# Performance work log

Measured on AMD Instinct MI355X. Metric: run time of the kernel, lower is better.

The kernel has to match this reference:

```python
import jax, jax.numpy as jnp
import numpy as np

D_IN = 1024
D_OUT = 1024


def setup_inputs() -> dict:
    key = jax.random.key(0)
    kx, kq, kk, kv = jax.random.split(key, 4)
    B, S = 4, 2048
    scale = 1.0 / np.sqrt(D_IN)
    return {
        "x": jax.random.normal(kx, (B, S, D_IN), dtype=jnp.float32),
        "Wq": jax.random.normal(kq, (D_IN, D_OUT), dtype=jnp.float32) * scale,
        "Wk": jax.random.normal(kk, (D_IN, D_OUT), dtype=jnp.float32) * scale,
        "Wv": jax.random.normal(kv, (D_IN, D_OUT), dtype=jnp.float32) * scale,
    }


def reference(x, Wq, Wk, Wv):
    # x: [B, S, D_in]; single-head causal attention (dropout=0 -> identity)
    q = jnp.einsum("bsd,de->bse", x, Wq)
    k = jnp.einsum("bsd,de->bse", x, Wk)
    v = jnp.einsum("bsd,de->bse", x, Wv)
    S = x.shape[1]
    d_k = k.shape[-1]
    scores = jnp.einsum("bqe,bke->bqk", q, k) / jnp.sqrt(jnp.float32(d_k))
    causal = jnp.tril(jnp.ones((S, S), dtype=bool))  # True = keep
    scores = jnp.where(causal, scores, -jnp.inf)
    weights = jax.nn.softmax(scores, axis=-1)
    return jnp.einsum("bqk,bke->bqe", weights, v)
```

## Files before the change

### kernel.cpp

```cpp
#include <hip/hip_runtime.h>

typedef unsigned short u16;
typedef __bf16 bf16x8_v __attribute__((ext_vector_type(8)));
typedef float f32x4 __attribute__((ext_vector_type(4)));

__device__ __forceinline__ u16 f2bf(float f) {
    unsigned u = __float_as_uint(f);
    unsigned r = u + 0x7fffu + ((u >> 16) & 1u);
    return (u16)(r >> 16);
}
__device__ __forceinline__ float bf2f(u16 h) {
    return __uint_as_float(((unsigned)h) << 16);
}

__device__ __forceinline__ void gll16(const u16* g, u16* l) {
    __builtin_amdgcn_global_load_lds(
        (const __attribute__((address_space(1))) void*)g,
        (__attribute__((address_space(3))) void*)l, 16, 0, 0);
}

#define EXP_SHIFT 12.0f

__device__ __forceinline__ float* srow_ptr(u16* Sb, int b, int i) {
    return (float*)((char*)Sb + (size_t)b * 8388608 +
                    ((i >> 9) << 12) + 2048 + ((size_t)(i & 511) << 2));
}

__global__ __launch_bounds__(256) void k_prep(const float* __restrict__ x,
                                              const float* __restrict__ Wq,
                                              const float* __restrict__ Wk,
                                              const float* __restrict__ Wv,
                                              u16* __restrict__ xb,
                                              u16* __restrict__ Wt3,
                                              float* __restrict__ out,
                                              u16* __restrict__ Sb) {
    __shared__ float tile[32][33];
    const int bid = blockIdx.x, tid = threadIdx.x;
    if (bid < 4096) {
        int i = (bid * 256 + tid) * 8;
        float4 a = *(const float4*)(x + i);
        float4 bb = *(const float4*)(x + i + 4);
        union { int4 p; u16 h[8]; } o;
        o.h[0] = f2bf(a.x);  o.h[1] = f2bf(a.y);  o.h[2] = f2bf(a.z);  o.h[3] = f2bf(a.w);
        o.h[4] = f2bf(bb.x); o.h[5] = f2bf(bb.y); o.h[6] = f2bf(bb.z); o.h[7] = f2bf(bb.w);
        *(int4*)(xb + i) = o.p;
    } else if (bid < 7168) {
        const int w = bid - 4096;
        const int z = w >> 10, rem = w & 1023;
        const int bx = rem & 31, by = rem >> 5;
        const float* W = (z == 0) ? Wq : (z == 1) ? Wk : Wv;
        u16* Wt = Wt3 + (size_t)z * 1024 * 1024;
        const int tx = tid & 31, ty = tid >> 5;
#pragma unroll
        for (int r = 0; r < 4; ++r)
            tile[ty + r * 8][tx] = W[(by * 32 + ty + r * 8) * 1024 + bx * 32 + tx];
        __syncthreads();
#pragma unroll
        for (int r = 0; r < 4; ++r)
            Wt[(bx * 32 + ty + r * 8) * 1024 + by * 32 + tx] =
                f2bf(tile[tx][ty + r * 8]);
    } else if (bid < 8192) {
        const int c = bid - 7168;
        int4 z4 = {0, 0, 0, 0};
        const int q0 = c * 1024 + tid * 4;
#pragma unroll
        for (int k = 0; k < 4; ++k) {
            const int q = q0 + k;
            const int b = q >> 18, off = q & 262143;
            *(int4*)(out + (size_t)b * 2097152 + 1048576 + (size_t)off * 4) = z4;
        }
    } else {
        const int chunk = tid >> 7;
        const int t = tid & 127;
#pragma unroll
        for (int c = 0; c < 8; ++c) {
            const int cc = c * 2 + chunk;
            char* p = (char*)Sb + (size_t)(cc >> 2) * 8388608 +
                      ((cc & 3) << 12) + 2048;
            int4 z4 = {0, 0, 0, 0};
            *(int4*)(p + t * 16) = z4;
        }
    }
}

__device__ __forceinline__ void gemm_core_nt(const u16* __restrict__ A,
                                             const u16* __restrict__ B,
                                             int lda, int ldb, int kLen,
                                             u16* smem, f32x4 acc[4][4]) {
    u16* As = smem;
    u16* Bs = smem + 128 * 64;
    const int tid = threadIdx.x;
    const int wave = tid >> 6;
    const int lane = tid & 63;
    const int rowA = tid >> 3;
    const int kcs  = (tid & 7) ^ (rowA & 7);
    const int row16 = lane & 15;
    const int quad = lane >> 4;
    const int sw = row16 & 7;
    const int wm = (wave >> 1) * 64;
    const int wn = (wave & 1) * 64;

#pragma unroll
    for (int i = 0; i < 4; ++i)
#pragma unroll
        for (int j = 0; j < 4; ++j) {
            f32x4 z = {0.f, 0.f, 0.f, 0.f};
            acc[i][j] = z;
        }

    const u16* Ag[4]; const u16* Bg[4];
    u16 *AsB[4], *BsB[4];
#pragma unroll
    for (int u = 0; u < 4; ++u) {
        Ag[u] = A + (size_t)(u * 32 + rowA) * lda + kcs * 8;
        Bg[u] = B + (size_t)(u * 32 + rowA) * ldb + kcs * 8;
        AsB[u] = As + (u * 256 + wave * 64) * 8;
        BsB[u] = Bs + (u * 256 + wave * 64) * 8;
    }

    const int ktiles = kLen >> 6;
    for (int kt = 0; kt < ktiles; ++kt) {
        __syncthreads();
#pragma unroll
        for (int u = 0; u < 4; ++u) gll16(Ag[u] + kt * 64, AsB[u]);
#pragma unroll
        for (int u = 0; u < 4; ++u) gll16(Bg[u] + kt * 64, BsB[u]);
        __syncthreads();
#pragma unroll
        for (int h = 0; h < 2; ++h) {
            bf16x8_v af[4], bfv[4];
            const int cp = (h * 4 + quad);
#pragma unroll
            for (int i = 0; i < 4; ++i)
                af[i] = *(const bf16x8_v*)(As + (wm + i * 16 + row16) * 64 +
                                           (cp ^ sw) * 8);
#pragma unroll
            for (int j = 0; j < 4; ++j)
                bfv[j] = *(const bf16x8_v*)(Bs + (wn + j * 16 + row16) * 64 +
                                            (cp ^ sw) * 8);
#pragma unroll
            for (int i = 0; i < 4; ++i)
#pragma unroll
                for (int j = 0; j < 4; ++j)
                    acc[i][j] = __builtin_amdgcn_mfma_f32_16x16x32_bf16(
                        af[i], bfv[j], acc[i][j], 0, 0, 0);
        }
    }
}

__device__ __forceinline__ void epi_bf16(const f32x4 acc[4][4], u16* smem,
                                         u16* __restrict__ g, int ldg) {
    const int tid = threadIdx.x;
    const int wave = tid >> 6, lane = tid & 63;
    const int row16 = lane & 15, quad = lane >> 4;
    u16* Ts = smem + wave * 2048;
#pragma unroll
    for (int jh = 0; jh < 2; ++jh) {
#pragma unroll
        for (int i = 0; i < 4; ++i)
#pragma unroll
            for (int jj = 0; jj < 2; ++jj) {
                const int j = jh * 2 + jj;
#pragma unroll
                for (int r = 0; r < 4; ++r)
                    Ts[(i * 16 + quad * 4 + r) * 32 + jj * 16 + row16] =
                        f2bf(acc[i][j][r]);
            }
#pragma unroll
        for (int s = 0; s < 4; ++s) {
            const int row = s * 16 + (lane >> 2);
            int4 val = *(const int4*)(Ts + row * 32 + (lane & 3) * 8);
            *(int4*)(g + (size_t)row * ldg + jh * 32 + (lane & 3) * 8) = val;
        }
    }
}

__device__ __forceinline__ void epi_vt(const f32x4 acc[4][4], u16* smem,
                                       u16* __restrict__ Vt, int m0w, int n0w) {
    const int tid = threadIdx.x;
    const int wave = tid >> 6, lane = tid & 63;
    const int row16 = lane & 15, quad = lane >> 4;
    const int b = m0w >> 11;
    const int sBase = m0w & 2047;
    u16* Ts = smem + wave * 4608;
#pragma unroll
    for (int p = 0; p < 2; ++p) {
#pragma unroll
        for (int i = 0; i < 4; ++i)
#pragma unroll
            for (int jj = 0; jj < 2; ++jj) {
                const int j = p * 2 + jj;
                union { unsigned long long d; u16 h[4]; } o;
#pragma unroll
                for (int r = 0; r < 4; ++r) o.h[r] = f2bf(acc[i][j][r]);
                *(unsigned long long*)(Ts + (jj * 16 + row16) * 72 +
                                       i * 16 + quad * 4) = o.d;
            }
#pragma unroll
        for (int rr = 0; rr < 4; ++rr) {
            const int ln = rr * 8 + (lane >> 3);
            const int ck = lane & 7;
            int4 val = *(const int4*)(Ts + ln * 72 + ck * 8);
            const int n = n0w + p * 32 + ln;
            *(int4*)(Vt + ((size_t)b * 1024 + n) * 2048 + sBase + ck * 8) = val;
        }
    }
}

__global__ __launch_bounds__(256, 3) void k_gemm_proj(const u16* __restrict__ X,
                                                      const u16* __restrict__ Wt3,
                                                      u16* __restrict__ Qb,
                                                      u16* __restrict__ Kb,
                                                      u16* __restrict__ Vt) {
    __shared__ u16 smem[18432];
    const int n0g = blockIdx.x * 128, m0 = blockIdx.y * 128;
    f32x4 acc[4][4];
    gemm_core_nt(X + (size_t)m0 * 1024, Wt3 + (size_t)n0g * 1024, 1024, 1024, 1024,
                 smem, acc);
    const int tid = threadIdx.x, wave = tid >> 6;
    const int wm = (wave >> 1) * 64, wn = (wave & 1) * 64;
    __syncthreads();
    if (n0g < 2048) {
        u16* Y = (n0g < 1024) ? Qb : Kb;
        const int n0 = n0g & 1023;
        epi_bf16(acc, smem, Y + (size_t)(m0 + wm) * 1024 + n0 + wn, 1024);
    } else {
        epi_vt(acc, smem, Vt, m0 + wm, (n0g - 2048) + wn);
    }
}

__global__ __launch_bounds__(256, 3) void k_gemm_scores(const u16* __restrict__ Q,
                                                        const u16* __restrict__ Kb,
                                                        u16* __restrict__ Sb) {
    __shared__ u16 smem[16384];
    int t = blockIdx.x, b = blockIdx.y;
    int mt = 0;
    while ((mt + 1) * (mt + 2) / 2 <= t) ++mt;
    int nt = t - mt * (mt + 1) / 2;
    const u16* Qp = Q + (size_t)b * 2048 * 1024 + (size_t)mt * 128 * 1024;
    const u16* Kp = Kb + (size_t)b * 2048 * 1024 + (size_t)nt * 128 * 1024;
    u16* Sp = Sb + (size_t)b * 2048 * 2048;
    f32x4 acc[4][4];
    gemm_core_nt(Qp, Kp, 1024, 1024, 1024, smem, acc);
    const int tid = threadIdx.x, wave = tid >> 6, lane = tid & 63;
    const int wm = (wave >> 1) * 64, wn = (wave & 1) * 64;
    const int row16 = lane & 15, quad = lane >> 4;
    const int mBase = mt * 128 + wm;
    const int nBase = nt * 128 + wn;
    u16* Ts = smem + wave * 2048;
    float rs[4][4];
#pragma unroll
    for (int i = 0; i < 4; ++i)
#pragma unroll
        for (int r = 0; r < 4; ++r) rs[i][r] = 0.f;

    __syncthreads();
#pragma unroll
    for (int jh = 0; jh < 2; ++jh) {
#pragma unroll
        for (int i = 0; i < 4; ++i)
#pragma unroll
            for (int jj = 0; jj < 2; ++jj) {
                const int j = jh * 2 + jj;
                const int n = nBase + jh * 32 + jj * 16 + row16;
#pragma unroll
                for (int r = 0; r < 4; ++r) {
                    const int m = mBase + i * 16 + quad * 4 + r;
                    float e = 0.f;
                    if (n <= m)
                        e = __expf(acc[i][j][r] * 0.03125f - EXP_SHIFT);
                    rs[i][r] += e;
                    Ts[(i * 16 + quad * 4 + r) * 32 + jj * 16 + row16] = f2bf(e);
                }
            }
#pragma unroll
        for (int s = 0; s < 4; ++s) {
            const int row = s * 16 + (lane >> 2);
            int4 val = *(const int4*)(Ts + row * 32 + (lane & 3) * 8);
            *(int4*)(Sp + (size_t)(mBase + row) * 2048 +
                     nBase + jh * 32 + (lane & 3) * 8) = val;
        }
    }
#pragma unroll
    for (int i = 0; i < 4; ++i)
#pragma unroll
        for (int r = 0; r < 4; ++r) {
            float s = rs[i][r];
#pragma unroll
            for (int off = 1; off < 16; off <<= 1) s += __shfl_xor(s, off);
            if (row16 == 0)
                atomicAdd(srow_ptr((u16*)Sb, b, mBase + i * 16 + quad * 4 + r), s);
        }
}

__global__ __launch_bounds__(256, 3) void k_gemm_pv(u16* __restrict__ P,
                                                    const u16* __restrict__ Vt,
                                                    float* __restrict__ O) {
    __shared__ u16 smem[16384];
    const int nt = blockIdx.x, b = blockIdx.z;
    const int y = blockIdx.y;
    int mt, c;
    if (y < 16) { mt = 8 + (y >> 1); c = y & 1; }
    else        { mt = y - 16;       c = 0; }
    const int kOff = c << 10;
    const int kLen = min(((mt + 1) << 7) - kOff, 1024);
    const u16* Pp = P + (size_t)b * 2048 * 2048 + (size_t)mt * 128 * 2048 + kOff;
    const u16* Vp = Vt + (size_t)b * 1024 * 2048 + (size_t)nt * 128 * 2048 + kOff;
    f32x4 acc[4][4];
    gemm_core_nt(Pp, Vp, 2048, 2048, kLen, smem, acc);
    float* Op = O + (size_t)b * 2048 * 1024;
    const int tid = threadIdx.x, wave = tid >> 6, lane = tid & 63;
    const int wm = (wave >> 1) * 64, wn = (wave & 1) * 64;
    const int row16 = lane & 15, quad = lane >> 4;
    float inv[4][4];
#pragma unroll
    for (int i = 0; i < 4; ++i)
#pragma unroll
        for (int r = 0; r < 4; ++r)
            inv[i][r] = 1.0f / *srow_ptr(P, b, mt * 128 + wm + i * 16 + quad * 4 + r);
    if (mt < 8) {
#pragma unroll
        for (int i = 0; i < 4; ++i)
#pragma unroll
            for (int j = 0; j < 4; ++j) {
                int m = mt * 128 + wm + i * 16 + quad * 4;
                int n = nt * 128 + wn + j * 16 + row16;
#pragma unroll
                for (int r = 0; r < 4; ++r)
                    Op[(size_t)(m + r) * 1024 + n] = acc[i][j][r] * inv[i][r];
            }
    } else {
#pragma unroll
        for (int i = 0; i < 4; ++i)
#pragma unroll
            for (int j = 0; j < 4; ++j) {
                int m = mt * 128 + wm + i * 16 + quad * 4;
                int n = nt * 128 + wn + j * 16 + row16;
#pragma unroll
                for (int r = 0; r < 4; ++r)
                    atomicAdd(&Op[(size_t)(m + r) * 1024 + n],
                              acc[i][j][r] * inv[i][r]);
            }
    }
}

extern "C" void kernel_launch(void* const* d_in, const int* in_sizes, int n_in,
                              void* d_out, int out_size, void* d_ws, size_t ws_size,
                              hipStream_t stream) {
    const float* x  = (const float*)d_in[0];
    const float* Wq = (const float*)d_in[1];
    const float* Wk = (const float*)d_in[2];
    const float* Wv = (const float*)d_in[3];
    float* out = (float*)d_out;
    char* ws = (char*)d_ws;

    u16* xb  = (u16*)(ws);
    u16* Wt3 = (u16*)(ws + (16u << 20));
    u16* Qb  = (u16*)(ws + (22u << 20));
    u16* Kb  = (u16*)(ws + (38u << 20));
    u16* Vt  = (u16*)(ws + (54u << 20));
    u16* Sb  = (u16*)(ws + (70u << 20));

    k_prep<<<8193, 256, 0, stream>>>(x, Wq, Wk, Wv, xb, Wt3, out, Sb);
    k_gemm_proj<<<dim3(24, 64), 256, 0, stream>>>(xb, Wt3, Qb, Kb, Vt);
    k_gemm_scores<<<dim3(136, 4), 256, 0, stream>>>(Qb, Kb, Sb);
    k_gemm_pv<<<dim3(8, 24, 4), 256, 0, stream>>>(Sb, Vt, out);
}
```

Measured before the change: 238.6 us.

## Replace atomic split-K accumulation in PV with partial buffers and combine kernel

The lower-half PV tiles (mt>=8) previously split K at a fixed 1024 boundary and accumulated into a zero-initialized output with float atomics. They now split K evenly into two halves, write each half to separate workspace buffers (reusing the Q/K regions), and a new combine kernel sums them into the output. This removes the zeroing pass in prep and the atomic traffic, and balances work between the two split blocks, at the cost of an extra kernel launch and an extra write/read of the partial tiles.

```diff
diff --git a/kernel.cpp b/kernel.cpp
--- a/kernel.cpp
+++ b/kernel.cpp
@@ -32,7 +32,6 @@
                                               const float* __restrict__ Wv,
                                               u16* __restrict__ xb,
                                               u16* __restrict__ Wt3,
-                                              float* __restrict__ out,
                                               u16* __restrict__ Sb) {
     __shared__ float tile[32][33];
     const int bid = blockIdx.x, tid = threadIdx.x;
@@ -59,16 +58,6 @@
         for (int r = 0; r < 4; ++r)
             Wt[(bx * 32 + ty + r * 8) * 1024 + by * 32 + tx] =
                 f2bf(tile[tx][ty + r * 8]);
-    } else if (bid < 8192) {
-        const int c = bid - 7168;
-        int4 z4 = {0, 0, 0, 0};
-        const int q0 = c * 1024 + tid * 4;
-#pragma unroll
-        for (int k = 0; k < 4; ++k) {
-            const int q = q0 + k;
-            const int b = q >> 18, off = q & 262143;
-            *(int4*)(out + (size_t)b * 2097152 + 1048576 + (size_t)off * 4) = z4;
-        }
     } else {
         const int chunk = tid >> 7;
         const int t = tid & 127;
@@ -295,20 +284,25 @@
 
 __global__ __launch_bounds__(256, 3) void k_gemm_pv(u16* __restrict__ P,
                                                     const u16* __restrict__ Vt,
-                                                    float* __restrict__ O) {
+                                                    float* __restrict__ O,
+                                                    float* __restrict__ P0,
+                                                    float* __restrict__ P1) {
     __shared__ u16 smem[16384];
     const int nt = blockIdx.x, b = blockIdx.z;
     const int y = blockIdx.y;
-    int mt, c;
-    if (y < 16) { mt = 8 + (y >> 1); c = y & 1; }
-    else        { mt = y - 16;       c = 0; }
-    const int kOff = c << 10;
-    const int kLen = min(((mt + 1) << 7) - kOff, 1024);
+    int mt, kOff, kLen;
+    if (y < 16) {
+        mt = 8 + (y >> 1);
+        const int half0 = (mt + 2) >> 1;
+        if ((y & 1) == 0) { kOff = 0;          kLen = half0 << 7; }
+        else              { kOff = half0 << 7; kLen = ((mt + 1) << 7) - kOff; }
+    } else {
+        mt = y - 16; kOff = 0; kLen = (mt + 1) << 7;
+    }
     const u16* Pp = P + (size_t)b * 2048 * 2048 + (size_t)mt * 128 * 2048 + kOff;
     const u16* Vp = Vt + (size_t)b * 1024 * 2048 + (size_t)nt * 128 * 2048 + kOff;
     f32x4 acc[4][4];
     gemm_core_nt(Pp, Vp, 2048, 2048, kLen, smem, acc);
-    float* Op = O + (size_t)b * 2048 * 1024;
     const int tid = threadIdx.x, wave = tid >> 6, lane = tid & 63;
     const int wm = (wave >> 1) * 64, wn = (wave & 1) * 64;
     const int row16 = lane & 15, quad = lane >> 4;
@@ -318,7 +312,8 @@
 #pragma unroll
         for (int r = 0; r < 4; ++r)
             inv[i][r] = 1.0f / *srow_ptr(P, b, mt * 128 + wm + i * 16 + quad * 4 + r);
-    if (mt < 8) {
+    if (y >= 16) {
+        float* Op = O + (size_t)b * 2048 * 1024;
 #pragma unroll
         for (int i = 0; i < 4; ++i)
 #pragma unroll
@@ -330,17 +325,40 @@
                     Op[(size_t)(m + r) * 1024 + n] = acc[i][j][r] * inv[i][r];
             }
     } else {
-#pragma unroll
-        for (int i = 0; i < 4; ++i)
-#pragma unroll
-            for (int j = 0; j < 4; ++j) {
-                int m = mt * 128 + wm + i * 16 + quad * 4;
-                int n = nt * 128 + wn + j * 16 + row16;
-#pragma unroll
-                for (int r = 0; r < 4; ++r)
-                    atomicAdd(&Op[(size_t)(m + r) * 1024 + n],
-                              acc[i][j][r] * inv[i][r]);
-            }
+        float* dst = ((y & 1) == 0 ? P0 : P1) +
+                     (size_t)(((b * 8 + (mt - 8)) * 8 + nt)) * 16384;
+#pragma unroll
+        for (int k = 0; k < 16; ++k) {
+            const int i = k >> 2, j = k & 3;
+            f32x4 sv;
+#pragma unroll
+            for (int r = 0; r < 4; ++r) sv[r] = acc[i][j][r] * inv[i][r];
+            *(f32x4*)(dst + (size_t)(k * 256 + tid) * 4) = sv;
+        }
+    }
+}
+
+__global__ __launch_bounds__(256) void k_pv_combine(const float* __restrict__ P0,
+                                                    const float* __restrict__ P1,
+                                                    float* __restrict__ O) {
+    const int t = blockIdx.x;
+    const int b = t >> 6, mt = 8 + ((t >> 3) & 7), nt = t & 7;
+    const int tid = threadIdx.x, wave = tid >> 6, lane = tid & 63;
+    const int wm = (wave >> 1) * 64, wn = (wave & 1) * 64;
+    const int row16 = lane & 15, quad = lane >> 4;
+    const float* p0 = P0 + (size_t)t * 16384;
+    const float* p1 = P1 + (size_t)t * 16384;
+    float* Op = O + (size_t)b * 2048 * 1024;
+#pragma unroll
+    for (int k = 0; k < 16; ++k) {
+        f32x4 a = *(const f32x4*)(p0 + (size_t)(k * 256 + tid) * 4);
+        f32x4 c = *(const f32x4*)(p1 + (size_t)(k * 256 + tid) * 4);
+        const int i = k >> 2, j = k & 3;
+        const int m = mt * 128 + wm + i * 16 + quad * 4;
+        const int n = nt * 128 + wn + j * 16 + row16;
+#pragma unroll
+        for (int r = 0; r < 4; ++r)
+            Op[(size_t)(m + r) * 1024 + n] = a[r] + c[r];
     }
 }
 
@@ -360,9 +378,12 @@
     u16* Kb  = (u16*)(ws + (38u << 20));
     u16* Vt  = (u16*)(ws + (54u << 20));
     u16* Sb  = (u16*)(ws + (70u << 20));
-
-    k_prep<<<8193, 256, 0, stream>>>(x, Wq, Wk, Wv, xb, Wt3, out, Sb);
+    float* P0 = (float*)Qb;
+    float* P1 = (float*)Kb;
+
+    k_prep<<<7169, 256, 0, stream>>>(x, Wq, Wk, Wv, xb, Wt3, Sb);
     k_gemm_proj<<<dim3(24, 64), 256, 0, stream>>>(xb, Wt3, Qb, Kb, Vt);
     k_gemm_scores<<<dim3(136, 4), 256, 0, stream>>>(Qb, Kb, Sb);
-    k_gemm_pv<<<dim3(8, 24, 4), 256, 0, stream>>>(Sb, Vt, out);
-}
+    k_gemm_pv<<<dim3(8, 24, 4), 256, 0, stream>>>(Sb, Vt, out, P0, P1);
+    k_pv_combine<<<256, 256, 0, stream>>>(P0, P1, out);
+}
```

Result: no change. 234.1 us (-1.9%).

## Drop split-K atomics in PV GEMM and raise occupancy bound to four

Applied to the files above, without the earlier changes.

The PV kernel no longer splits the lower-half row tiles into two K chunks accumulated with atomics. Each block now owns a full row tile, and the heaviest tiles are launched first. This removes the output zero-fill in the prep kernel and the atomic adds, at the cost of fewer blocks and longer tail blocks. Launch bounds for the scores and PV kernels are raised to request four blocks per CU, which may constrain registers.

```diff
diff --git a/kernel.cpp b/kernel.cpp
--- a/kernel.cpp
+++ b/kernel.cpp
@@ -32,7 +32,6 @@
                                               const float* __restrict__ Wv,
                                               u16* __restrict__ xb,
                                               u16* __restrict__ Wt3,
-                                              float* __restrict__ out,
                                               u16* __restrict__ Sb) {
     __shared__ float tile[32][33];
     const int bid = blockIdx.x, tid = threadIdx.x;
@@ -59,16 +58,6 @@
         for (int r = 0; r < 4; ++r)
             Wt[(bx * 32 + ty + r * 8) * 1024 + by * 32 + tx] =
                 f2bf(tile[tx][ty + r * 8]);
-    } else if (bid < 8192) {
-        const int c = bid - 7168;
-        int4 z4 = {0, 0, 0, 0};
-        const int q0 = c * 1024 + tid * 4;
-#pragma unroll
-        for (int k = 0; k < 4; ++k) {
-            const int q = q0 + k;
-            const int b = q >> 18, off = q & 262143;
-            *(int4*)(out + (size_t)b * 2097152 + 1048576 + (size_t)off * 4) = z4;
-        }
     } else {
         const int chunk = tid >> 7;
         const int t = tid & 127;
@@ -229,7 +218,7 @@
     }
 }
 
-__global__ __launch_bounds__(256, 3) void k_gemm_scores(const u16* __restrict__ Q,
+__global__ __launch_bounds__(256, 4) void k_gemm_scores(const u16* __restrict__ Q,
                                                         const u16* __restrict__ Kb,
                                                         u16* __restrict__ Sb) {
     __shared__ u16 smem[16384];
@@ -293,21 +282,15 @@
         }
 }
 
-__global__ __launch_bounds__(256, 3) void k_gemm_pv(u16* __restrict__ P,
+__global__ __launch_bounds__(256, 4) void k_gemm_pv(u16* __restrict__ P,
                                                     const u16* __restrict__ Vt,
                                                     float* __restrict__ O) {
     __shared__ u16 smem[16384];
-    const int nt = blockIdx.x, b = blockIdx.z;
-    const int y = blockIdx.y;
-    int mt, c;
-    if (y < 16) { mt = 8 + (y >> 1); c = y & 1; }
-    else        { mt = y - 16;       c = 0; }
-    const int kOff = c << 10;
-    const int kLen = min(((mt + 1) << 7) - kOff, 1024);
-    const u16* Pp = P + (size_t)b * 2048 * 2048 + (size_t)mt * 128 * 2048 + kOff;
-    const u16* Vp = Vt + (size_t)b * 1024 * 2048 + (size_t)nt * 128 * 2048 + kOff;
+    const int nt = blockIdx.x, mt = 15 - blockIdx.y, b = blockIdx.z;
+    const u16* Pp = P + (size_t)b * 2048 * 2048 + (size_t)mt * 128 * 2048;
+    const u16* Vp = Vt + (size_t)b * 1024 * 2048 + (size_t)nt * 128 * 2048;
     f32x4 acc[4][4];
-    gemm_core_nt(Pp, Vp, 2048, 2048, kLen, smem, acc);
+    gemm_core_nt(Pp, Vp, 2048, 2048, (mt + 1) * 128, smem, acc);
     float* Op = O + (size_t)b * 2048 * 1024;
     const int tid = threadIdx.x, wave = tid >> 6, lane = tid & 63;
     const int wm = (wave >> 1) * 64, wn = (wave & 1) * 64;
@@ -318,30 +301,16 @@
 #pragma unroll
         for (int r = 0; r < 4; ++r)
             inv[i][r] = 1.0f / *srow_ptr(P, b, mt * 128 + wm + i * 16 + quad * 4 + r);
-    if (mt < 8) {
-#pragma unroll
-        for (int i = 0; i < 4; ++i)
-#pragma unroll
-            for (int j = 0; j < 4; ++j) {
-                int m = mt * 128 + wm + i * 16 + quad * 4;
-                int n = nt * 128 + wn + j * 16 + row16;
-#pragma unroll
-                for (int r = 0; r < 4; ++r)
-                    Op[(size_t)(m + r) * 1024 + n] = acc[i][j][r] * inv[i][r];
-            }
-    } else {
-#pragma unroll
-        for (int i = 0; i < 4; ++i)
-#pragma unroll
-            for (int j = 0; j < 4; ++j) {
-                int m = mt * 128 + wm + i * 16 + quad * 4;
-                int n = nt * 128 + wn + j * 16 + row16;
-#pragma unroll
-                for (int r = 0; r < 4; ++r)
-                    atomicAdd(&Op[(size_t)(m + r) * 1024 + n],
-                              acc[i][j][r] * inv[i][r]);
-            }
-    }
+#pragma unroll
+    for (int i = 0; i < 4; ++i)
+#pragma unroll
+        for (int j = 0; j < 4; ++j) {
+            int m = mt * 128 + wm + i * 16 + quad * 4;
+            int n = nt * 128 + wn + j * 16 + row16;
+#pragma unroll
+            for (int r = 0; r < 4; ++r)
+                Op[(size_t)(m + r) * 1024 + n] = acc[i][j][r] * inv[i][r];
+        }
 }
 
 extern "C" void kernel_launch(void* const* d_in, const int* in_sizes, int n_in,
@@ -361,8 +330,8 @@
     u16* Vt  = (u16*)(ws + (54u << 20));
     u16* Sb  = (u16*)(ws + (70u << 20));
 
-    k_prep<<<8193, 256, 0, stream>>>(x, Wq, Wk, Wv, xb, Wt3, out, Sb);
+    k_prep<<<7169, 256, 0, stream>>>(x, Wq, Wk, Wv, xb, Wt3, Sb);
     k_gemm_proj<<<dim3(24, 64), 256, 0, stream>>>(xb, Wt3, Qb, Kb, Vt);
     k_gemm_scores<<<dim3(136, 4), 256, 0, stream>>>(Qb, Kb, Sb);
-    k_gemm_pv<<<dim3(8, 24, 4), 256, 0, stream>>>(Sb, Vt, out);
-}
+    k_gemm_pv<<<dim3(8, 16, 4), 256, 0, stream>>>(Sb, Vt, out);
+}
```

Measured after the change: 225.6 us. 1.06x faster.
